# Performance work log

Measured on AMD Instinct MI355X. Metric: run time of the kernel, lower is better.

Reference implementation:

```python
import jax, jax.numpy as jnp
import numpy as np

B, C, H, W = 4, 64, 128, 128
O, K = 64, 3
STRIDE, PAD = 1, 1
K2 = K * K


def conv2d(x, w, b):
    out = jax.lax.conv_general_dilated(
        x, w, (STRIDE, STRIDE), [(PAD, PAD), (PAD, PAD)],
        dimension_numbers=('NCHW', 'OIHW', 'NCHW'))
    return out + b[None, :, None, None]


def setup_inputs() -> dict:
    key = jax.random.key(0)
    ks = jax.random.split(key, 6)
    return {
        'x': jax.random.normal(ks[0], (B, C, H, W), jnp.float32),
        'offset_w': jax.random.normal(ks[1], (2 * K2, C, K, K), jnp.float32) * 0.01,
        'offset_b': jax.random.normal(ks[2], (2 * K2,), jnp.float32) * 0.01,
        'mask_w': jax.random.normal(ks[3], (K2, C, K, K), jnp.float32) * 0.01,
        'mask_b': jnp.zeros((K2,), jnp.float32),
        'deform_w': jax.random.normal(ks[4], (O, C, K, K), jnp.float32) * (1.0 / np.sqrt(C * K2)),
        'deform_b': jax.random.normal(ks[5], (O,), jnp.float32) * 0.01,
    }


def _deform_conv(x, offset, mask, w, b):
    Bn, Cn, Hin, Win = x.shape
    Ho, Wo = offset.shape[2], offset.shape[3]
    off = offset.reshape(Bn, K2, 2, Ho, Wo)
    ky = jnp.repeat(jnp.arange(K), K)   # kernel row offset per location k
    kx = jnp.tile(jnp.arange(K), K)     # kernel col offset per location k
    yo = jnp.arange(Ho) * STRIDE - PAD
    xo = jnp.arange(Wo) * STRIDE - PAD
    # sampling positions [B,K2,Ho,Wo]
    py = off[:, :, 0] + ky[None, :, None, None] + yo[None, None, :, None]
    px = off[:, :, 1] + kx[None, :, None, None] + xo[None, None, None, :]
    y0 = jnp.floor(py)
    x0 = jnp.floor(px)
    wy1 = py - y0  # fractional weights
    wx1 = px - x0
    y0i = y0.astype(jnp.int32)
    x0i = x0.astype(jnp.int32)
    x_flat = x.reshape(Bn, Cn, Hin * Win)

    def corner(yi, xi, wgt):
        valid = (yi >= 0) & (yi < Hin) & (xi >= 0) & (xi < Win)
        yc = jnp.clip(yi, 0, Hin - 1)
        xc = jnp.clip(xi, 0, Win - 1)
        idx = (yc * Win + xc).reshape(Bn, -1)
        g = jnp.take_along_axis(x_flat, idx[:, None, :], axis=2)
        g = g.reshape(Bn, Cn, K2, Ho, Wo)
        return g * (wgt * valid)[:, None]

    val = (corner(y0i, x0i, (1 - wy1) * (1 - wx1))
           + corner(y0i, x0i + 1, (1 - wy1) * wx1)
           + corner(y0i + 1, x0i, wy1 * (1 - wx1))
           + corner(y0i + 1, x0i + 1, wy1 * wx1))
    val = val * mask[:, None]  # modulate, broadcast over channels
    out = jnp.einsum('bckhw,ock->bohw', val, w.reshape(w.shape[0], Cn, K2))
    return out + b[None, :, None, None]


def reference(x, offset_w, offset_b, mask_w, mask_b, deform_w, deform_b):
    offset = conv2d(x, offset_w, offset_b)
    mask = jax.nn.sigmoid(conv2d(x, mask_w, mask_b))
    return _deform_conv(x, offset, mask, deform_w, deform_b)
```

## Files before the change

### kernel.cpp

```cpp
#include <hip/hip_runtime.h>
#include <hip/hip_bf16.h>
#include <math.h>

#define BB 4
#define CC 64
#define HH 128
#define WW 128
#define HW 16384
#define CHW (CC*HW)

typedef __bf16 bf16;
typedef __attribute__((ext_vector_type(8))) __bf16 bf16x8;
typedef __attribute__((ext_vector_type(4))) __bf16 bf16x4;
typedef __attribute__((ext_vector_type(4))) float f32x4;
typedef __attribute__((ext_vector_type(4))) unsigned short u16x4;

#define MFMA(a, b, c) __builtin_amdgcn_mfma_f32_16x16x32_bf16((a), (b), (c), 0, 0, 0)

__global__ __launch_bounds__(256) void k_pre(const float* __restrict__ x,
        bf16* __restrict__ xt,
        const float* __restrict__ dw, const float* __restrict__ ow,
        const float* __restrict__ mw,
        bf16* __restrict__ wfd_hi, bf16* __restrict__ wfd_lo,
        bf16* __restrict__ wfo_hi, bf16* __restrict__ wfo_lo) {
    __shared__ float tile[64][65];
    if (blockIdx.x < 1024) {
        int b    = blockIdx.x >> 8;
        int s0   = (blockIdx.x & 255) * 64;
        int lane = threadIdx.x & 63;
        int w    = threadIdx.x >> 6;
        const float* xb = x + (size_t)b * CHW;
        #pragma unroll
        for (int r = 0; r < 16; ++r) {
            int c = w * 16 + r;
            tile[c][lane] = xb[(size_t)c * HW + s0 + lane];
        }
        __syncthreads();
        bf16* xtb = xt + (size_t)b * CHW;
        #pragma unroll
        for (int r = 0; r < 16; ++r) {
            int si = w * 16 + r;
            xtb[(size_t)(s0 + si) * 64 + lane] = (bf16)tile[lane][si];
        }
    } else {
        int idx = (blockIdx.x - 1024) * 256 + threadIdx.x;
        if (idx < 36864) {
            int j    = idx & 7;
            int lane = (idx >> 3) & 63;
            int ks   = (idx >> 9) % 18;
            int nt   = idx / (512 * 18);
            int n    = nt * 16 + (lane & 15);
            int kglob = ks * 32 + (lane >> 4) * 8 + j;
            int kk = kglob >> 6, c = kglob & 63;
            float w = dw[(n * 64 + c) * 9 + kk];
            bf16 h = (bf16)w;
            wfd_hi[idx] = h;
            wfd_lo[idx] = (bf16)(w - (float)h);
        } else {
            int idx2 = idx - 36864;
            int j    = idx2 & 7;
            int lane = (idx2 >> 3) & 63;
            int ks   = (idx2 >> 9) % 18;
            int nt   = idx2 / (512 * 18);
            int ch   = nt * 16 + (lane & 15);
            int kglob = ks * 32 + (lane >> 4) * 8 + j;
            int kk = kglob >> 6, c = kglob & 63;
            float w = 0.0f;
            if (ch < 18)      w = ow[(ch * 64 + c) * 9 + kk];
            else if (ch < 27) w = mw[((ch - 18) * 64 + c) * 9 + kk];
            bf16 h = (bf16)w;
            wfo_hi[idx2] = h;
            wfo_lo[idx2] = (bf16)(w - (float)h);
        }
    }
}

__global__ __launch_bounds__(256) void k_fused(const bf16* __restrict__ xt,
        const bf16* __restrict__ wfo_hi, const bf16* __restrict__ wfo_lo,
        const bf16* __restrict__ wfd_hi,
        const float* __restrict__ ob, const float* __restrict__ mb,
        const float* __restrict__ db, float* __restrict__ out) {
    __shared__ __align__(16) bf16 a_s[18 * 64 * 8];
    __shared__ float om_s[27 * 64];
    __shared__ __align__(8) bf16 sampw[576 * 4];
    __shared__ __align__(8) unsigned short sampo[576 * 4];

    int pos0 = blockIdx.x * 64;
    int wo0 = pos0 & 127;
    int ho  = (pos0 >> 7) & 127;
    int b   = pos0 >> 14;
    int t = threadIdx.x, wave = t >> 6, lane = t & 63;
    int m = lane & 15, g = lane >> 4;
    const bf16* xtb = xt + (size_t)b * CHW;

    {
        int st = wave;
        f32x4 acc0 = {0.f, 0.f, 0.f, 0.f};
        f32x4 acc1 = {0.f, 0.f, 0.f, 0.f};
        const bf16x8* bh0 = (const bf16x8*)wfo_hi + lane;
        const bf16x8* bl0 = (const bf16x8*)wfo_lo + lane;
        const bf16x8* bh1 = (const bf16x8*)wfo_hi + 18 * 64 + lane;
        const bf16x8* bl1 = (const bf16x8*)wfo_lo + 18 * 64 + lane;
        #pragma unroll
        for (int kk = 0; kk < 9; ++kk) {
            int y  = ho + kk / 3 - 1;
            int xx = wo0 + st * 16 + m + (kk % 3) - 1;
            bf16x8 ae = {};
            bf16x8 ao = {};
            if ((unsigned)y < 128u && (unsigned)xx < 128u) {
                const bf16* bp = xtb + ((size_t)(y * 128 + xx) << 6);
                ae = *(const bf16x8*)(bp + g * 8);
                ao = *(const bf16x8*)(bp + 32 + g * 8);
            }
            int ks0 = 2 * kk, ks1 = 2 * kk + 1;
            acc0 = MFMA(ae, bh0[ks0 * 64], acc0);
            acc0 = MFMA(ae, bl0[ks0 * 64], acc0);
            acc0 = MFMA(ao, bh0[ks1 * 64], acc0);
            acc0 = MFMA(ao, bl0[ks1 * 64], acc0);
            acc1 = MFMA(ae, bh1[ks0 * 64], acc1);
            acc1 = MFMA(ae, bl1[ks0 * 64], acc1);
            acc1 = MFMA(ao, bh1[ks1 * 64], acc1);
            acc1 = MFMA(ao, bl1[ks1 * 64], acc1);
        }
        int p64 = st * 16 + g * 4;
        float bias0 = ob[m];
        #pragma unroll
        for (int r = 0; r < 4; ++r)
            om_s[m * 64 + p64 + r] = acc0[r] + bias0;
        int ch1 = 16 + m;
        if (ch1 < 27) {
            float bias1 = (ch1 < 18) ? ob[ch1] : mb[ch1 - 18];
            #pragma unroll
            for (int r = 0; r < 4; ++r) {
                float v = acc1[r] + bias1;
                if (ch1 >= 18) v = 1.0f / (1.0f + __expf(-v));
                om_s[ch1 * 64 + p64 + r] = v;
            }
        }
    }
    __syncthreads();

    for (int task = t; task < 576; task += 256) {
        int p64 = task / 9, k = task - p64 * 9;
        float dy = om_s[(2 * k) * 64 + p64];
        float dx = om_s[(2 * k + 1) * 64 + p64];
        float mk = om_s[(18 + k) * 64 + p64];
        float py = (float)(ho - 1 + k / 3) + dy;
        float px = (float)(wo0 + p64 - 1 + (k % 3)) + dx;
        float y0f = floorf(py), x0f = floorf(px);
        float fy = py - y0f, fx = px - x0f;
        int y0 = (int)y0f, x0 = (int)x0f;
        int y1 = y0 + 1,  x1 = x0 + 1;
        bool vy0 = (unsigned)y0 < 128u, vy1 = (unsigned)y1 < 128u;
        bool vx0 = (unsigned)x0 < 128u, vx1 = (unsigned)x1 < 128u;
        int y0c = min(max(y0, 0), 127), y1c = min(max(y1, 0), 127);
        int x0c = min(max(x0, 0), 127), x1c = min(max(x1, 0), 127);
        bf16x4 wv;
        wv.x = (bf16)((vy0 && vx0) ? mk * (1.f - fy) * (1.f - fx) : 0.f);
        wv.y = (bf16)((vy0 && vx1) ? mk * (1.f - fy) * fx         : 0.f);
        wv.z = (bf16)((vy1 && vx0) ? mk * fy * (1.f - fx)         : 0.f);
        wv.w = (bf16)((vy1 && vx1) ? mk * fy * fx                 : 0.f);
        u16x4 ov;
        ov.x = (unsigned short)(y0c * 128 + x0c);
        ov.y = (unsigned short)(y0c * 128 + x1c);
        ov.z = (unsigned short)(y1c * 128 + x0c);
        ov.w = (unsigned short)(y1c * 128 + x1c);
        *(bf16x4*)&sampw[task * 4] = wv;
        *(u16x4*)&sampo[task * 4] = ov;
    }
    __syncthreads();

    const bf16x8* bhd = (const bf16x8*)wfd_hi + (size_t)wave * 18 * 64 + lane;
    int c4 = m * 4;
    int p = wave * 4 + g;
    int gch = (c4 & 31) >> 3;
    int kpar = c4 >> 5;
    int fle = ((m ^ g) + (g << 4)) * 8;
    int flo = ((m ^ g ^ 4) + (g << 4)) * 8;

    for (int st = 0; st < 4; ++st) {
        int taskbase = (st * 16 + p) * 9;
        #pragma unroll
        for (int kk = 0; kk < 9; ++kk) {
            int task = taskbase + kk;
            bf16x4 wb = *(const bf16x4*)&sampw[task * 4];
            u16x4  o4 = *(const u16x4*)&sampo[task * 4];
            bf16x4 v00 = *(const bf16x4*)&xtb[((int)o4.x << 6) + c4];
            bf16x4 v01 = *(const bf16x4*)&xtb[((int)o4.y << 6) + c4];
            bf16x4 v10 = *(const bf16x4*)&xtb[((int)o4.z << 6) + c4];
            bf16x4 v11 = *(const bf16x4*)&xtb[((int)o4.w << 6) + c4];
            float w00 = (float)wb.x, w01 = (float)wb.y;
            float w10 = (float)wb.z, w11 = (float)wb.w;
            float r0 = w00 * (float)v00.x + w01 * (float)v01.x + w10 * (float)v10.x + w11 * (float)v11.x;
            float r1 = w00 * (float)v00.y + w01 * (float)v01.y + w10 * (float)v10.y + w11 * (float)v11.y;
            float r2 = w00 * (float)v00.z + w01 * (float)v01.z + w10 * (float)v10.z + w11 * (float)v11.z;
            float r3 = w00 * (float)v00.w + w01 * (float)v01.w + w10 * (float)v10.w + w11 * (float)v11.w;
            int ks = 2 * kk + kpar;
            int fl = (p ^ gch ^ ((ks & 1) << 2)) + (gch << 4);
            bf16x4 hv = {(bf16)r0, (bf16)r1, (bf16)r2, (bf16)r3};
            *(bf16x4*)((char*)a_s + (((ks * 64 + fl) << 4) + ((c4 & 7) << 1))) = hv;
        }
        __syncthreads();

        f32x4 acc = {0.f, 0.f, 0.f, 0.f};
        #pragma unroll
        for (int kk = 0; kk < 9; ++kk) {
            bf16x8 a0 = *(const bf16x8*)&a_s[(2 * kk) * 512 + fle];
            bf16x8 a1 = *(const bf16x8*)&a_s[(2 * kk + 1) * 512 + flo];
            acc = MFMA(a0, bhd[(2 * kk) * 64], acc);
            acc = MFMA(a1, bhd[(2 * kk + 1) * 64], acc);
        }
        int o = wave * 16 + m;
        float bias = db[o];
        float4 vv = {acc[0] + bias, acc[1] + bias, acc[2] + bias, acc[3] + bias};
        *(float4*)&out[((size_t)(b * 64 + o)) * HW + ho * 128 + wo0 + st * 16 + g * 4] = vv;
        if (st < 3) __syncthreads();
    }
}

extern "C" void kernel_launch(void* const* d_in, const int* in_sizes, int n_in,
                              void* d_out, int out_size, void* d_ws, size_t ws_size,
                              hipStream_t stream) {
    const float* x   = (const float*)d_in[0];
    const float* ow  = (const float*)d_in[1];
    const float* ob  = (const float*)d_in[2];
    const float* mw  = (const float*)d_in[3];
    const float* mb  = (const float*)d_in[4];
    const float* dw  = (const float*)d_in[5];
    const float* db  = (const float*)d_in[6];
    float* out = (float*)d_out;

    bf16* xt = (bf16*)d_ws;
    bf16* wfd_hi = xt + (size_t)BB * HW * CC;
    bf16* wfd_lo = wfd_hi + 36864;
    bf16* wfo_hi = wfd_lo + 36864;
    bf16* wfo_lo = wfo_hi + 18432;

    k_pre<<<1024 + 216, 256, 0, stream>>>(x, xt, dw, ow, mw, wfd_hi, wfd_lo, wfo_hi, wfo_lo);
    k_fused<<<(BB * HW) / 64, 256, 0, stream>>>(xt, wfo_hi, wfo_lo, wfd_hi, ob, mb, db, out);
}
```

Baseline: 128.3 us.

## Make each wave own 16 positions end-to-end, build MFMA A-fragments in registers

The fused kernel now gives each wave its own 16 output positions through offset conv, sampling-table build and deform GEMM. Barriers are replaced with wave-local LDS waits, and the bilinear-sampled values are formed directly as MFMA A operands in registers, dropping the shared a_s staging buffer. Each wave computes all 64 output channels with four accumulators. Blocks are also remapped across batch/rows for locality, and the transpose pre-kernel now writes 16-byte vectors instead of scalar bf16 stores. This raises register pressure and reloads all deform weight fragments per wave.

```diff
diff --git a/kernel.cpp b/kernel.cpp
--- a/kernel.cpp
+++ b/kernel.cpp
@@ -38,9 +38,13 @@
         __syncthreads();
         bf16* xtb = xt + (size_t)b * CHW;
         #pragma unroll
-        for (int r = 0; r < 16; ++r) {
-            int si = w * 16 + r;
-            xtb[(size_t)(s0 + si) * 64 + lane] = (bf16)tile[lane][si];
+        for (int it = 0; it < 2; ++it) {
+            int task = it * 256 + threadIdx.x;
+            int s = task >> 3, ch0 = (task & 7) * 8;
+            bf16x8 v;
+            #pragma unroll
+            for (int j = 0; j < 8; ++j) v[j] = (bf16)tile[ch0 + j][s];
+            *(bf16x8*)&xtb[(size_t)(s0 + s) * 64 + ch0] = v;
         }
     } else {
         int idx = (blockIdx.x - 1024) * 256 + threadIdx.x;
@@ -80,21 +84,24 @@
         const bf16* __restrict__ wfd_hi,
         const float* __restrict__ ob, const float* __restrict__ mb,
         const float* __restrict__ db, float* __restrict__ out) {
-    __shared__ __align__(16) bf16 a_s[18 * 64 * 8];
-    __shared__ float om_s[27 * 64];
-    __shared__ __align__(8) bf16 sampw[576 * 4];
-    __shared__ __align__(8) unsigned short sampo[576 * 4];
-
-    int pos0 = blockIdx.x * 64;
+    __shared__ __align__(16) float om_s[4 * 27 * 16];
+    __shared__ __align__(8)  bf16 sampw[4 * 144 * 4];
+    __shared__ __align__(8)  unsigned short sampo[4 * 144 * 4];
+
+    int bid = (blockIdx.x & 7) * 128 + (blockIdx.x >> 3);
+    int pos0 = bid * 64;
     int wo0 = pos0 & 127;
     int ho  = (pos0 >> 7) & 127;
     int b   = pos0 >> 14;
     int t = threadIdx.x, wave = t >> 6, lane = t & 63;
     int m = lane & 15, g = lane >> 4;
+    int st = wave;
     const bf16* xtb = xt + (size_t)b * CHW;
+    float* omw = om_s + wave * 27 * 16;
+    bf16* swv = sampw + wave * 144 * 4;
+    unsigned short* sov = sampo + wave * 144 * 4;
 
     {
-        int st = wave;
         f32x4 acc0 = {0.f, 0.f, 0.f, 0.f};
         f32x4 acc1 = {0.f, 0.f, 0.f, 0.f};
         const bf16x8* bh0 = (const bf16x8*)wfo_hi + lane;
@@ -122,99 +129,104 @@
             acc1 = MFMA(ao, bh1[ks1 * 64], acc1);
             acc1 = MFMA(ao, bl1[ks1 * 64], acc1);
         }
-        int p64 = st * 16 + g * 4;
         float bias0 = ob[m];
-        #pragma unroll
-        for (int r = 0; r < 4; ++r)
-            om_s[m * 64 + p64 + r] = acc0[r] + bias0;
+        f32x4 v0;
+        #pragma unroll
+        for (int r = 0; r < 4; ++r) v0[r] = acc0[r] + bias0;
+        *(f32x4*)&omw[m * 16 + g * 4] = v0;
         int ch1 = 16 + m;
         if (ch1 < 27) {
             float bias1 = (ch1 < 18) ? ob[ch1] : mb[ch1 - 18];
+            f32x4 v1;
             #pragma unroll
             for (int r = 0; r < 4; ++r) {
                 float v = acc1[r] + bias1;
                 if (ch1 >= 18) v = 1.0f / (1.0f + __expf(-v));
-                om_s[ch1 * 64 + p64 + r] = v;
+                v1[r] = v;
             }
-        }
-    }
-    __syncthreads();
-
-    for (int task = t; task < 576; task += 256) {
-        int p64 = task / 9, k = task - p64 * 9;
-        float dy = om_s[(2 * k) * 64 + p64];
-        float dx = om_s[(2 * k + 1) * 64 + p64];
-        float mk = om_s[(18 + k) * 64 + p64];
-        float py = (float)(ho - 1 + k / 3) + dy;
-        float px = (float)(wo0 + p64 - 1 + (k % 3)) + dx;
-        float y0f = floorf(py), x0f = floorf(px);
-        float fy = py - y0f, fx = px - x0f;
-        int y0 = (int)y0f, x0 = (int)x0f;
-        int y1 = y0 + 1,  x1 = x0 + 1;
-        bool vy0 = (unsigned)y0 < 128u, vy1 = (unsigned)y1 < 128u;
-        bool vx0 = (unsigned)x0 < 128u, vx1 = (unsigned)x1 < 128u;
-        int y0c = min(max(y0, 0), 127), y1c = min(max(y1, 0), 127);
-        int x0c = min(max(x0, 0), 127), x1c = min(max(x1, 0), 127);
-        bf16x4 wv;
-        wv.x = (bf16)((vy0 && vx0) ? mk * (1.f - fy) * (1.f - fx) : 0.f);
-        wv.y = (bf16)((vy0 && vx1) ? mk * (1.f - fy) * fx         : 0.f);
-        wv.z = (bf16)((vy1 && vx0) ? mk * fy * (1.f - fx)         : 0.f);
-        wv.w = (bf16)((vy1 && vx1) ? mk * fy * fx                 : 0.f);
-        u16x4 ov;
-        ov.x = (unsigned short)(y0c * 128 + x0c);
-        ov.y = (unsigned short)(y0c * 128 + x1c);
-        ov.z = (unsigned short)(y1c * 128 + x0c);
-        ov.w = (unsigned short)(y1c * 128 + x1c);
-        *(bf16x4*)&sampw[task * 4] = wv;
-        *(u16x4*)&sampo[task * 4] = ov;
-    }
-    __syncthreads();
-
-    const bf16x8* bhd = (const bf16x8*)wfd_hi + (size_t)wave * 18 * 64 + lane;
-    int c4 = m * 4;
-    int p = wave * 4 + g;
-    int gch = (c4 & 31) >> 3;
-    int kpar = c4 >> 5;
-    int fle = ((m ^ g) + (g << 4)) * 8;
-    int flo = ((m ^ g ^ 4) + (g << 4)) * 8;
-
-    for (int st = 0; st < 4; ++st) {
-        int taskbase = (st * 16 + p) * 9;
-        #pragma unroll
-        for (int kk = 0; kk < 9; ++kk) {
-            int task = taskbase + kk;
-            bf16x4 wb = *(const bf16x4*)&sampw[task * 4];
-            u16x4  o4 = *(const u16x4*)&sampo[task * 4];
-            bf16x4 v00 = *(const bf16x4*)&xtb[((int)o4.x << 6) + c4];
-            bf16x4 v01 = *(const bf16x4*)&xtb[((int)o4.y << 6) + c4];
-            bf16x4 v10 = *(const bf16x4*)&xtb[((int)o4.z << 6) + c4];
-            bf16x4 v11 = *(const bf16x4*)&xtb[((int)o4.w << 6) + c4];
-            float w00 = (float)wb.x, w01 = (float)wb.y;
-            float w10 = (float)wb.z, w11 = (float)wb.w;
-            float r0 = w00 * (float)v00.x + w01 * (float)v01.x + w10 * (float)v10.x + w11 * (float)v11.x;
-            float r1 = w00 * (float)v00.y + w01 * (float)v01.y + w10 * (float)v10.y + w11 * (float)v11.y;
-            float r2 = w00 * (float)v00.z + w01 * (float)v01.z + w10 * (float)v10.z + w11 * (float)v11.z;
-            float r3 = w00 * (float)v00.w + w01 * (float)v01.w + w10 * (float)v10.w + w11 * (float)v11.w;
-            int ks = 2 * kk + kpar;
-            int fl = (p ^ gch ^ ((ks & 1) << 2)) + (gch << 4);
-            bf16x4 hv = {(bf16)r0, (bf16)r1, (bf16)r2, (bf16)r3};
-            *(bf16x4*)((char*)a_s + (((ks * 64 + fl) << 4) + ((c4 & 7) << 1))) = hv;
-        }
-        __syncthreads();
-
-        f32x4 acc = {0.f, 0.f, 0.f, 0.f};
-        #pragma unroll
-        for (int kk = 0; kk < 9; ++kk) {
-            bf16x8 a0 = *(const bf16x8*)&a_s[(2 * kk) * 512 + fle];
-            bf16x8 a1 = *(const bf16x8*)&a_s[(2 * kk + 1) * 512 + flo];
-            acc = MFMA(a0, bhd[(2 * kk) * 64], acc);
-            acc = MFMA(a1, bhd[(2 * kk + 1) * 64], acc);
-        }
-        int o = wave * 16 + m;
+            *(f32x4*)&omw[ch1 * 16 + g * 4] = v1;
+        }
+    }
+    asm volatile("s_waitcnt lgkmcnt(0)" ::: "memory");
+
+    #pragma unroll
+    for (int i = 0; i < 3; ++i) {
+        int task = i * 64 + lane;
+        if (task < 144) {
+            int p = task / 9, k = task - p * 9;
+            float dy = omw[(2 * k) * 16 + p];
+            float dx = omw[(2 * k + 1) * 16 + p];
+            float mk = omw[(18 + k) * 16 + p];
+            float py = (float)(ho - 1 + k / 3) + dy;
+            float px = (float)(wo0 + st * 16 + p - 1 + (k % 3)) + dx;
+            float y0f = floorf(py), x0f = floorf(px);
+            float fy = py - y0f, fx = px - x0f;
+            int y0 = (int)y0f, x0 = (int)x0f;
+            int y1 = y0 + 1,  x1 = x0 + 1;
+            bool vy0 = (unsigned)y0 < 128u, vy1 = (unsigned)y1 < 128u;
+            bool vx0 = (unsigned)x0 < 128u, vx1 = (unsigned)x1 < 128u;
+            int y0c = min(max(y0, 0), 127), y1c = min(max(y1, 0), 127);
+            int x0c = min(max(x0, 0), 127), x1c = min(max(x1, 0), 127);
+            bf16x4 wv;
+            wv.x = (bf16)((vy0 && vx0) ? mk * (1.f - fy) * (1.f - fx) : 0.f);
+            wv.y = (bf16)((vy0 && vx1) ? mk * (1.f - fy) * fx         : 0.f);
+            wv.z = (bf16)((vy1 && vx0) ? mk * fy * (1.f - fx)         : 0.f);
+            wv.w = (bf16)((vy1 && vx1) ? mk * fy * fx                 : 0.f);
+            u16x4 ov;
+            ov.x = (unsigned short)(y0c * 128 + x0c);
+            ov.y = (unsigned short)(y0c * 128 + x1c);
+            ov.z = (unsigned short)(y1c * 128 + x0c);
+            ov.w = (unsigned short)(y1c * 128 + x1c);
+            *(bf16x4*)&swv[task * 4] = wv;
+            *(u16x4*)&sov[task * 4] = ov;
+        }
+    }
+    asm volatile("s_waitcnt lgkmcnt(0)" ::: "memory");
+
+    const bf16x8* bfd = (const bf16x8*)wfd_hi + lane;
+    f32x4 acc[4];
+    #pragma unroll
+    for (int nt = 0; nt < 4; ++nt) acc[nt] = (f32x4){0.f, 0.f, 0.f, 0.f};
+    int sb = m * 9 * 4;
+    #pragma unroll 3
+    for (int kk = 0; kk < 9; ++kk) {
+        bf16x4 wb = *(const bf16x4*)&swv[sb + kk * 4];
+        u16x4  o4 = *(const u16x4*)&sov[sb + kk * 4];
+        const bf16* p00 = xtb + (((int)o4.x) << 6) + g * 8;
+        const bf16* p01 = xtb + (((int)o4.y) << 6) + g * 8;
+        const bf16* p10 = xtb + (((int)o4.z) << 6) + g * 8;
+        const bf16* p11 = xtb + (((int)o4.w) << 6) + g * 8;
+        bf16x8 v00a = *(const bf16x8*)p00, v00b = *(const bf16x8*)(p00 + 32);
+        bf16x8 v01a = *(const bf16x8*)p01, v01b = *(const bf16x8*)(p01 + 32);
+        bf16x8 v10a = *(const bf16x8*)p10, v10b = *(const bf16x8*)(p10 + 32);
+        bf16x8 v11a = *(const bf16x8*)p11, v11b = *(const bf16x8*)(p11 + 32);
+        float w00 = (float)wb.x, w01 = (float)wb.y;
+        float w10 = (float)wb.z, w11 = (float)wb.w;
+        bf16x8 af0, af1;
+        #pragma unroll
+        for (int j = 0; j < 8; ++j) {
+            af0[j] = (bf16)(w00 * (float)v00a[j] + w01 * (float)v01a[j]
+                          + w10 * (float)v10a[j] + w11 * (float)v11a[j]);
+            af1[j] = (bf16)(w00 * (float)v00b[j] + w01 * (float)v01b[j]
+                          + w10 * (float)v10b[j] + w11 * (float)v11b[j]);
+        }
+        int ks0 = 2 * kk, ks1 = 2 * kk + 1;
+        acc[0] = MFMA(af0, bfd[(0 * 18 + ks0) * 64], acc[0]);
+        acc[0] = MFMA(af1, bfd[(0 * 18 + ks1) * 64], acc[0]);
+        acc[1] = MFMA(af0, bfd[(1 * 18 + ks0) * 64], acc[1]);
+        acc[1] = MFMA(af1, bfd[(1 * 18 + ks1) * 64], acc[1]);
+        acc[2] = MFMA(af0, bfd[(2 * 18 + ks0) * 64], acc[2]);
+        acc[2] = MFMA(af1, bfd[(2 * 18 + ks1) * 64], acc[2]);
+        acc[3] = MFMA(af0, bfd[(3 * 18 + ks0) * 64], acc[3]);
+        acc[3] = MFMA(af1, bfd[(3 * 18 + ks1) * 64], acc[3]);
+    }
+    #pragma unroll
+    for (int nt = 0; nt < 4; ++nt) {
+        int o = nt * 16 + m;
         float bias = db[o];
-        float4 vv = {acc[0] + bias, acc[1] + bias, acc[2] + bias, acc[3] + bias};
+        float4 vv = {acc[nt][0] + bias, acc[nt][1] + bias,
+                     acc[nt][2] + bias, acc[nt][3] + bias};
         *(float4*)&out[((size_t)(b * 64 + o)) * HW + ho * 128 + wo0 + st * 16 + g * 4] = vv;
-        if (st < 3) __syncthreads();
     }
 }
 
@@ -226,8 +238,8 @@
     const float* ob  = (const float*)d_in[2];
     const float* mw  = (const float*)d_in[3];
     const float* mb  = (const float*)d_in[4];
+    const float* db  = (const float*)d_in[6];
     const float* dw  = (const float*)d_in[5];
-    const float* db  = (const float*)d_in[6];
     float* out = (float*)d_out;
 
     bf16* xt = (bf16*)d_ws;
```

Result: slower. 138.9 us (+8.3%).

## Widen gather to 8 channels, double A tile, remap blocks, vectorize transpose

Applied to the files above, without the earlier changes.

The sampling gather now has each thread handle 8 channels with 16-byte loads. Two A tiles are built per pass, so the four sub-tiles need two barrier rounds instead of four, and MFMA sections get a raised wave priority. Block indices are remapped across an 8-way interleave, which changes which positions run together and so cache locality. The pre-kernel transpose now writes bf16x8 vectors instead of scalars. In exchange, shared memory doubles for the A buffer and register pressure rises.

```diff
diff --git a/kernel.cpp b/kernel.cpp
--- a/kernel.cpp
+++ b/kernel.cpp
@@ -38,9 +38,13 @@
         __syncthreads();
         bf16* xtb = xt + (size_t)b * CHW;
         #pragma unroll
-        for (int r = 0; r < 16; ++r) {
-            int si = w * 16 + r;
-            xtb[(size_t)(s0 + si) * 64 + lane] = (bf16)tile[lane][si];
+        for (int it = 0; it < 2; ++it) {
+            int task = it * 256 + threadIdx.x;
+            int s = task >> 3, ch0 = (task & 7) * 8;
+            bf16x8 v;
+            #pragma unroll
+            for (int j = 0; j < 8; ++j) v[j] = (bf16)tile[ch0 + j][s];
+            *(bf16x8*)&xtb[(size_t)(s0 + s) * 64 + ch0] = v;
         }
     } else {
         int idx = (blockIdx.x - 1024) * 256 + threadIdx.x;
@@ -80,12 +84,13 @@
         const bf16* __restrict__ wfd_hi,
         const float* __restrict__ ob, const float* __restrict__ mb,
         const float* __restrict__ db, float* __restrict__ out) {
-    __shared__ __align__(16) bf16 a_s[18 * 64 * 8];
+    __shared__ __align__(16) bf16 a_s2[2][18 * 64 * 8];
     __shared__ float om_s[27 * 64];
     __shared__ __align__(8) bf16 sampw[576 * 4];
     __shared__ __align__(8) unsigned short sampo[576 * 4];
 
-    int pos0 = blockIdx.x * 64;
+    int bid = (blockIdx.x & 7) * 128 + (blockIdx.x >> 3);
+    int pos0 = bid * 64;
     int wo0 = pos0 & 127;
     int ho  = (pos0 >> 7) & 127;
     int b   = pos0 >> 14;
@@ -171,50 +176,63 @@
     __syncthreads();
 
     const bf16x8* bhd = (const bf16x8*)wfd_hi + (size_t)wave * 18 * 64 + lane;
-    int c4 = m * 4;
-    int p = wave * 4 + g;
-    int gch = (c4 & 31) >> 3;
-    int kpar = c4 >> 5;
     int fle = ((m ^ g) + (g << 4)) * 8;
     int flo = ((m ^ g ^ 4) + (g << 4)) * 8;
-
-    for (int st = 0; st < 4; ++st) {
-        int taskbase = (st * 16 + p) * 9;
+    int half = t >> 7;
+    int prow = (t >> 3) & 15;
+    int c8   = (t & 7) * 8;
+    int kpar = c8 >> 5;
+    int gch  = (c8 & 31) >> 3;
+    int flw  = (prow ^ gch ^ (kpar << 2)) + (gch << 4);
+    char* abw = (char*)&a_s2[half][0] + (flw << 4);
+
+    #pragma unroll
+    for (int sp = 0; sp < 2; ++sp) {
+        int stc = sp * 2 + half;
+        int taskbase = (stc * 16 + prow) * 9;
         #pragma unroll
         for (int kk = 0; kk < 9; ++kk) {
             int task = taskbase + kk;
             bf16x4 wb = *(const bf16x4*)&sampw[task * 4];
             u16x4  o4 = *(const u16x4*)&sampo[task * 4];
-            bf16x4 v00 = *(const bf16x4*)&xtb[((int)o4.x << 6) + c4];
-            bf16x4 v01 = *(const bf16x4*)&xtb[((int)o4.y << 6) + c4];
-            bf16x4 v10 = *(const bf16x4*)&xtb[((int)o4.z << 6) + c4];
-            bf16x4 v11 = *(const bf16x4*)&xtb[((int)o4.w << 6) + c4];
+            bf16x8 v00 = *(const bf16x8*)&xtb[((int)o4.x << 6) + c8];
+            bf16x8 v01 = *(const bf16x8*)&xtb[((int)o4.y << 6) + c8];
+            bf16x8 v10 = *(const bf16x8*)&xtb[((int)o4.z << 6) + c8];
+            bf16x8 v11 = *(const bf16x8*)&xtb[((int)o4.w << 6) + c8];
             float w00 = (float)wb.x, w01 = (float)wb.y;
             float w10 = (float)wb.z, w11 = (float)wb.w;
-            float r0 = w00 * (float)v00.x + w01 * (float)v01.x + w10 * (float)v10.x + w11 * (float)v11.x;
-            float r1 = w00 * (float)v00.y + w01 * (float)v01.y + w10 * (float)v10.y + w11 * (float)v11.y;
-            float r2 = w00 * (float)v00.z + w01 * (float)v01.z + w10 * (float)v10.z + w11 * (float)v11.z;
-            float r3 = w00 * (float)v00.w + w01 * (float)v01.w + w10 * (float)v10.w + w11 * (float)v11.w;
+            bf16x8 hv;
+            #pragma unroll
+            for (int j = 0; j < 8; ++j) {
+                float r = w00 * (float)v00[j] + w01 * (float)v01[j]
+                        + w10 * (float)v10[j] + w11 * (float)v11[j];
+                hv[j] = (bf16)r;
+            }
             int ks = 2 * kk + kpar;
-            int fl = (p ^ gch ^ ((ks & 1) << 2)) + (gch << 4);
-            bf16x4 hv = {(bf16)r0, (bf16)r1, (bf16)r2, (bf16)r3};
-            *(bf16x4*)((char*)a_s + (((ks * 64 + fl) << 4) + ((c4 & 7) << 1))) = hv;
+            *(bf16x8*)(abw + (ks << 10)) = hv;
         }
         __syncthreads();
 
-        f32x4 acc = {0.f, 0.f, 0.f, 0.f};
-        #pragma unroll
-        for (int kk = 0; kk < 9; ++kk) {
-            bf16x8 a0 = *(const bf16x8*)&a_s[(2 * kk) * 512 + fle];
-            bf16x8 a1 = *(const bf16x8*)&a_s[(2 * kk + 1) * 512 + flo];
-            acc = MFMA(a0, bhd[(2 * kk) * 64], acc);
-            acc = MFMA(a1, bhd[(2 * kk + 1) * 64], acc);
-        }
-        int o = wave * 16 + m;
-        float bias = db[o];
-        float4 vv = {acc[0] + bias, acc[1] + bias, acc[2] + bias, acc[3] + bias};
-        *(float4*)&out[((size_t)(b * 64 + o)) * HW + ho * 128 + wo0 + st * 16 + g * 4] = vv;
-        if (st < 3) __syncthreads();
+        #pragma unroll
+        for (int h2 = 0; h2 < 2; ++h2) {
+            int st = sp * 2 + h2;
+            const bf16* ab = &a_s2[h2][0];
+            f32x4 acc = {0.f, 0.f, 0.f, 0.f};
+            __builtin_amdgcn_s_setprio(1);
+            #pragma unroll
+            for (int kk = 0; kk < 9; ++kk) {
+                bf16x8 a0 = *(const bf16x8*)&ab[(2 * kk) * 512 + fle];
+                bf16x8 a1 = *(const bf16x8*)&ab[(2 * kk + 1) * 512 + flo];
+                acc = MFMA(a0, bhd[(2 * kk) * 64], acc);
+                acc = MFMA(a1, bhd[(2 * kk + 1) * 64], acc);
+            }
+            __builtin_amdgcn_s_setprio(0);
+            int o = wave * 16 + m;
+            float bias = db[o];
+            float4 vv = {acc[0] + bias, acc[1] + bias, acc[2] + bias, acc[3] + bias};
+            *(float4*)&out[((size_t)(b * 64 + o)) * HW + ho * 128 + wo0 + st * 16 + g * 4] = vv;
+        }
+        if (sp == 0) __syncthreads();
     }
 }
 
```

New measurement: 121.7 us. -5.1%, faster.
